# Optimization experiments

Hardware: AMD Instinct MI355X
Metric: run time of the kernel (lower is better)

The kernel has to match this reference:

```python
import jax, jax.numpy as jnp
import numpy as np

N, E, IN, H, F = 50000, 800000, 128, 4, 32
NEG_SLOPE = 0.2


def setup_inputs() -> dict:
    key = jax.random.key(0)
    ks = jax.random.split(key, 10)
    feat = jax.random.normal(ks[0], (N, IN), dtype=jnp.float32)
    s = 0.05  # small scale to keep activations stable
    W_src_mut = jax.random.normal(ks[1], (IN, H * F), dtype=jnp.float32) * s
    W_dst_mut = jax.random.normal(ks[2], (IN, H * F), dtype=jnp.float32) * s
    W_self = jax.random.normal(ks[3], (IN, H * F), dtype=jnp.float32) * s
    W_lin = jax.random.normal(ks[4], (IN, F), dtype=jnp.float32) * s
    attn = jax.random.normal(ks[5], (H, F), dtype=jnp.float32) * s
    src = jax.random.randint(ks[6], (E,), 0, N, dtype=jnp.int64)
    dst = jax.random.randint(ks[7], (E,), 0, N, dtype=jnp.int64)
    return {
        'feat': feat,
        'W_src_mut': W_src_mut, 'b_src_mut': jnp.zeros((H * F,), jnp.float32),
        'W_dst_mut': W_dst_mut, 'b_dst_mut': jnp.zeros((H * F,), jnp.float32),
        'W_self': W_self, 'b_self': jnp.zeros((H * F,), jnp.float32),
        'W_lin': W_lin, 'b_lin': jnp.zeros((F,), jnp.float32),
        'attn': attn, 'src': src, 'dst': dst,
    }


def reference(feat, W_src_mut, b_src_mut, W_dst_mut, b_dst_mut,
              W_self, b_self, W_lin, b_lin, attn, src, dst):
    n = feat.shape[0]
    # node projections -> [N, H, F]
    el_mut = (feat @ W_src_mut + b_src_mut).reshape(n, H, F)
    er_mut = (feat @ W_dst_mut + b_dst_mut).reshape(n, H, F)
    el_self = (feat @ W_self + b_self).reshape(n, H, F)
    feat_lin = (feat @ W_lin + b_lin)[:, None, :]  # [N, 1, F]
    # edge attention scores: u_add_v -> leaky_relu -> dot with attn -> [E, H]
    e = jax.nn.leaky_relu(el_mut[src] + er_mut[dst], NEG_SLOPE)
    s = jnp.einsum('ehf,hf->eh', e, attn)
    # edge softmax over incoming edges of each dst node
    smax = jax.ops.segment_max(s, dst, num_segments=n)
    ex = jnp.exp(s - smax[dst])
    denom = jax.ops.segment_sum(ex, dst, num_segments=n)
    a = ex / denom[dst]  # [E, H]
    # weighted aggregation: u_mul_e + sum over dst
    m = el_self[src] * a[:, :, None]  # [E, H, F]
    ft = jax.ops.segment_sum(m, dst, num_segments=n)  # [N, H, F]
    # concat along head axis: [N, H+1, F]
    return jnp.concatenate([feat_lin, ft], axis=1)
```

## Files before the change

### kernel.cpp

```cpp
#include <hip/hip_runtime.h>
#include <hip/hip_bf16.h>

#define NN 50000
#define EE 800000
#define INF_ 128
#define HH 4
#define FF 32
#define HF 128
#define OUTC 160
#define NEG_SLOPE 0.2f

#define SCAN_B 196

typedef __attribute__((ext_vector_type(8))) short short8;
typedef __attribute__((ext_vector_type(4))) float f32x4;
typedef _Float16 f16x2 __attribute__((ext_vector_type(2)));
typedef float fl2 __attribute__((ext_vector_type(2)));

__device__ __forceinline__ unsigned short f2bf(float f) {
    union { float f; unsigned u; } in; in.f = f;
    unsigned u = in.u;
    u += 0x7fffu + ((u >> 16) & 1u);
    return (unsigned short)(u >> 16);
}
__device__ __forceinline__ unsigned short f2h(float f) {
    _Float16 h = (_Float16)f;
    return __builtin_bit_cast(unsigned short, h);
}
__device__ __forceinline__ f16x2 bch(unsigned u) {
    return __builtin_bit_cast(f16x2, u);
}
__device__ __forceinline__ f16x2 habs2(f16x2 v) {
    unsigned u = __builtin_bit_cast(unsigned, v) & 0x7FFF7FFFu;
    return __builtin_bit_cast(f16x2, u);
}

__device__ __forceinline__ void async_cp16(const void* g, void* l) {
    __builtin_amdgcn_global_load_lds(
        (const __attribute__((address_space(1))) void*)g,
        (__attribute__((address_space(3))) void*)l, 16, 0, 0);
}

__global__ __launch_bounds__(256) void prep_w(
    const float* __restrict__ W0, const float* __restrict__ b0,
    const float* __restrict__ W1, const float* __restrict__ b1,
    const float* __restrict__ W2, const float* __restrict__ b2,
    const float* __restrict__ W3, const float* __restrict__ b3,
    const float* __restrict__ attn,
    unsigned short* __restrict__ WbT, float* __restrict__ biasc,
    unsigned short* __restrict__ ath)
{
    int idx = blockIdx.x * 256 + threadIdx.x;
    int n = idx >> 7, k = idx & 127;
    float v;
    if (n < 128)      v = W0[k * 128 + n];
    else if (n < 256) v = W1[k * 128 + (n - 128)];
    else if (n < 384) v = W2[k * 128 + (n - 256)];
    else              v = W3[k * 32  + (n - 384)];
    int phys = (((k >> 3) ^ (n & 15)) << 3) | (k & 7);
    WbT[n * 128 + phys] = f2bf(v);
    if (idx < 416) {
        float bv;
        if (idx < 128)      bv = b0[idx];
        else if (idx < 256) bv = b1[idx - 128];
        else if (idx < 384) bv = b2[idx - 256];
        else                bv = b3[idx - 384];
        biasc[idx] = bv;
    }
    if (idx < 128) ath[idx] = f2h(attn[idx]);
}

__global__ __launch_bounds__(256) void scan_bsum(
    const int* __restrict__ counts, int* __restrict__ bsum)
{
    __shared__ int sh[256];
    int t = threadIdx.x;
    int idx = blockIdx.x * 256 + t;
    sh[t] = (idx < NN) ? counts[idx] : 0;
    __syncthreads();
    #pragma unroll
    for (int off = 128; off > 0; off >>= 1) {
        if (t < off) sh[t] += sh[t + off];
        __syncthreads();
    }
    if (t == 0) bsum[blockIdx.x] = sh[0];
}

__global__ __launch_bounds__(256) void scan_top(
    const int* __restrict__ bsum, int* __restrict__ bprefix)
{
    __shared__ int sh[256];
    int t = threadIdx.x;
    int v = (t < SCAN_B) ? bsum[t] : 0;
    sh[t] = v;
    __syncthreads();
    #pragma unroll
    for (int off = 1; off < 256; off <<= 1) {
        int u = (t >= off) ? sh[t - off] : 0;
        __syncthreads();
        sh[t] += u;
        __syncthreads();
    }
    if (t < SCAN_B) bprefix[t] = sh[t] - v;
}

__global__ __launch_bounds__(256) void scan_final(
    const int* __restrict__ counts, const int* __restrict__ bprefix,
    int* __restrict__ offsets)
{
    __shared__ int sh[256];
    int t = threadIdx.x;
    int idx = blockIdx.x * 256 + t;
    int v = (idx < NN) ? counts[idx] : 0;
    sh[t] = v;
    __syncthreads();
    #pragma unroll
    for (int off = 1; off < 256; off <<= 1) {
        int u = (t >= off) ? sh[t - off] : 0;
        __syncthreads();
        sh[t] += u;
        __syncthreads();
    }
    if (idx < NN) offsets[idx] = sh[t] - v + bprefix[blockIdx.x];
}

__global__ void scatter_kernel(const int* __restrict__ src, const int* __restrict__ dst,
                               const int* __restrict__ offsets, const int* __restrict__ rank,
                               int* __restrict__ srcbuck)
{
    int e = blockIdx.x * blockDim.x + threadIdx.x;
    if (e < EE) srcbuck[offsets[dst[e]] + rank[e]] = src[e];
}


template<int CPR, int CSTR, int CA0>
__device__ __forceinline__ void copy_out(
    const unsigned short* Cs, int row0, int tid,
    unsigned short* __restrict__ muth, unsigned short* __restrict__ erh,
    unsigned short* __restrict__ selfh)
{
    for (int c = tid; c < 64 * CPR; c += 256) {
        int row = c / CPR, c16 = c - row * CPR;
        int grow = row0 + row;
        if (grow >= NN) continue;
        uint4 v = *(const uint4*)(Cs + row * CSTR + c16 * 8);
        int ca = CA0 + c16;
        if (ca < 16)      *(uint4*)(muth  + (size_t)grow * 128 + ca * 8) = v;
        else if (ca < 32) *(uint4*)(erh   + (size_t)grow * 128 + (ca - 16) * 8) = v;
        else              *(uint4*)(selfh + (size_t)grow * 128 + (ca - 32) * 8) = v;
    }
}

__global__ __launch_bounds__(256) void gemm_hist(
    const float* __restrict__ feat,
    const unsigned short* __restrict__ WbT,
    const float* __restrict__ biasc,
    const int* __restrict__ dst,
    unsigned short* __restrict__ muth, unsigned short* __restrict__ selfh,
    unsigned short* __restrict__ erh, float* __restrict__ out,
    int* __restrict__ counts, int* __restrict__ rank)
{
    __shared__ __align__(16) char lds[16384 + 28672];
    unsigned short* As = (unsigned short*)lds;
    unsigned short* Bs = (unsigned short*)(lds + 16384);
    unsigned short* Cs = (unsigned short*)lds;

    const int tid  = threadIdx.x;
    const int wv   = tid >> 6;
    const int lane = tid & 63;
    const int row0 = blockIdx.x * 64;
    const int yb   = blockIdx.y;

    {
        int e = (yb * 782 + blockIdx.x) * 256 + tid;
        if (e < EE) rank[e] = atomicAdd(&counts[dst[e]], 1);
    }

    const int ntile = (yb & 1) ? 6 : 7;
    const int base  = (yb == 0) ? 0 : (yb == 1) ? 112 : (yb == 2) ? 208 : 320;

    {
        const char* g = (const char*)(WbT + (size_t)base * 128);
        #pragma unroll
        for (int it = 0; it < 7; ++it) {
            if (it < ntile) {
                int seg = wv * ntile + it;
                async_cp16(g + seg * 1024 + lane * 16, (char*)Bs + seg * 1024);
            }
        }
    }
    {
        #pragma unroll
        for (int i = 0; i < 4; ++i) {
            int idx = i * 256 + tid;
            int r = idx >> 4, c = idx & 15;
            int grow = row0 + r;
            float4 v0 = make_float4(0.f, 0.f, 0.f, 0.f), v1 = v0;
            if (grow < NN) {
                const float4* fp = (const float4*)(feat + (size_t)grow * 128 + c * 8);
                v0 = fp[0]; v1 = fp[1];
            }
            uint4 o;
            o.x = (unsigned)f2bf(v0.x) | ((unsigned)f2bf(v0.y) << 16);
            o.y = (unsigned)f2bf(v0.z) | ((unsigned)f2bf(v0.w) << 16);
            o.z = (unsigned)f2bf(v1.x) | ((unsigned)f2bf(v1.y) << 16);
            o.w = (unsigned)f2bf(v1.z) | ((unsigned)f2bf(v1.w) << 16);
            *(uint4*)(As + r * 128 + ((c ^ (r & 15)) << 3)) = o;
        }
    }
    __syncthreads();

    const int m16  = lane & 15;
    const int quad = lane >> 4;

    f32x4 acc[7];
    #pragma unroll
    for (int t = 0; t < 7; ++t) acc[t] = (f32x4){0.f, 0.f, 0.f, 0.f};

    short8 afr[4];
    {
        const unsigned short* Ab = As + (wv * 16 + m16) * 128;
        #pragma unroll
        for (int ks = 0; ks < 4; ++ks)
            afr[ks] = *(const short8*)(Ab + (((ks * 4 + quad) ^ m16) << 3));
    }

    #pragma unroll
    for (int t = 0; t < 7; ++t) {
        if (t >= ntile) break;
        const unsigned short* Bb = Bs + (t * 16 + m16) * 128;
        #pragma unroll
        for (int ks = 0; ks < 4; ++ks) {
            short8 bfr = *(const short8*)(Bb + (((ks * 4 + quad) ^ m16) << 3));
            acc[t] = __builtin_amdgcn_mfma_f32_16x16x32_bf16(afr[ks], bfr, acc[t], 0, 0, 0);
        }
    }

    if (yb == 3) {
        #pragma unroll
        for (int t = 4; t < 6; ++t) {
            int col = 320 + t * 16 + m16;
            float bb = biasc[col];
            #pragma unroll
            for (int r = 0; r < 4; ++r) {
                int grow = row0 + wv * 16 + quad * 4 + r;
                if (grow < NN) out[(size_t)grow * OUTC + (col - 384)] = acc[t][r] + bb;
            }
        }
    }

    __syncthreads();

    const int ntf  = (yb == 3) ? 4 : ntile;
    const int cstr = (yb & 1) ? ((yb == 1) ? 104 : 72) : 120;
    #pragma unroll
    for (int t = 0; t < 7; ++t) {
        if (t >= ntf) break;
        int col = base + t * 16 + m16;
        float bb = biasc[col];
        #pragma unroll
        for (int r = 0; r < 4; ++r) {
            int lrow = wv * 16 + quad * 4 + r;
            Cs[lrow * cstr + t * 16 + m16] = f2h(acc[t][r] + bb);
        }
    }
    __syncthreads();

    if (yb == 0)      copy_out<14, 120, 0 >(Cs, row0, tid, muth, erh, selfh);
    else if (yb == 1) copy_out<12, 104, 14>(Cs, row0, tid, muth, erh, selfh);
    else if (yb == 2) copy_out<14, 120, 26>(Cs, row0, tid, muth, erh, selfh);
    else              copy_out<8,  72,  40>(Cs, row0, tid, muth, erh, selfh);
}

__device__ __forceinline__ void edgeP(
    const uint2 m, const uint2 sf, const f16x2 er01, const f16x2 er23,
    const f16x2 at01, const f16x2 at23,
    float& l, float& a0, float& a1, float& a2, float& a3)
{
    f16x2 z01 = bch(m.x) + er01;
    f16x2 z23 = bch(m.y) + er23;
    float s1 = __builtin_amdgcn_fdot2(at01, z01, 0.f, false);
    s1 = __builtin_amdgcn_fdot2(at23, z23, s1, false);
    float s2 = __builtin_amdgcn_fdot2(at01, habs2(z01), 0.f, false);
    s2 = __builtin_amdgcn_fdot2(at23, habs2(z23), s2, false);
    float s = fmaf(0.6f, s1, 0.4f * s2);
    s += __shfl_xor(s, 1, 64);
    s += __shfl_xor(s, 2, 64);
    s += __shfl_xor(s, 4, 64);
    float p = __expf(s);
    l += p;
    fl2 c01 = __builtin_convertvector(bch(sf.x), fl2);
    fl2 c23 = __builtin_convertvector(bch(sf.y), fl2);
    a0 = fmaf(p, c01.x, a0);
    a1 = fmaf(p, c01.y, a1);
    a2 = fmaf(p, c23.x, a2);
    a3 = fmaf(p, c23.y, a3);
}

__global__ __launch_bounds__(256) void node_agg5(
    const unsigned short* __restrict__ muth,
    const unsigned short* __restrict__ selfh,
    const unsigned short* __restrict__ erh,
    const unsigned short* __restrict__ ath,
    const int* __restrict__ offsets, const int* __restrict__ counts,
    const int* __restrict__ srcbuck, float* __restrict__ out)
{
    const int n = blockIdx.x * 4 + (threadIdx.x >> 6);
    if (n >= NN) return;
    const int lane = threadIdx.x & 63;
    const int half = lane >> 5;
    const int li   = lane & 31;

    uint2 aw = *(const uint2*)(ath + li * 4);
    uint2 ew = *(const uint2*)(erh + (size_t)n * HF + li * 4);
    const f16x2 at01 = bch(aw.x), at23 = bch(aw.y);
    const f16x2 er01 = bch(ew.x), er23 = bch(ew.y);

    const int beg = offsets[n];
    const int deg = counts[n];
    const int cnt0 = (deg + 1) >> 1;
    const int st  = beg + (half ? cnt0 : 0);
    const int cnt = half ? (deg - cnt0) : cnt0;

    float l = 0.f, a0 = 0.f, a1 = 0.f, a2 = 0.f, a3 = 0.f;

    int k = 0;
    for (; k + 4 <= cnt; k += 4) {
        int i0 = srcbuck[st + k];
        int i1 = srcbuck[st + k + 1];
        int i2 = srcbuck[st + k + 2];
        int i3 = srcbuck[st + k + 3];
        uint2 m0 = *(const uint2*)(muth + (size_t)i0 * HF + li * 4);
        uint2 m1 = *(const uint2*)(muth + (size_t)i1 * HF + li * 4);
        uint2 m2 = *(const uint2*)(muth + (size_t)i2 * HF + li * 4);
        uint2 m3 = *(const uint2*)(muth + (size_t)i3 * HF + li * 4);
        uint2 s0 = *(const uint2*)(selfh + (size_t)i0 * HF + li * 4);
        uint2 s1 = *(const uint2*)(selfh + (size_t)i1 * HF + li * 4);
        uint2 s2 = *(const uint2*)(selfh + (size_t)i2 * HF + li * 4);
        uint2 s3 = *(const uint2*)(selfh + (size_t)i3 * HF + li * 4);
        edgeP(m0, s0, er01, er23, at01, at23, l, a0, a1, a2, a3);
        edgeP(m1, s1, er01, er23, at01, at23, l, a0, a1, a2, a3);
        edgeP(m2, s2, er01, er23, at01, at23, l, a0, a1, a2, a3);
        edgeP(m3, s3, er01, er23, at01, at23, l, a0, a1, a2, a3);
    }
    for (; k < cnt; ++k) {
        int i0 = srcbuck[st + k];
        uint2 m0 = *(const uint2*)(muth + (size_t)i0 * HF + li * 4);
        uint2 s0 = *(const uint2*)(selfh + (size_t)i0 * HF + li * 4);
        edgeP(m0, s0, er01, er23, at01, at23, l, a0, a1, a2, a3);
    }

    l  += __shfl_xor(l,  32, 64);
    a0 += __shfl_xor(a0, 32, 64);
    a1 += __shfl_xor(a1, 32, 64);
    a2 += __shfl_xor(a2, 32, 64);
    a3 += __shfl_xor(a3, 32, 64);

    if (half == 0) {
        float inv = (l > 0.f) ? __frcp_rn(l) : 0.f;
        float4 r = make_float4(a0 * inv, a1 * inv, a2 * inv, a3 * inv);
        *(float4*)(out + (size_t)n * OUTC + FF + li * 4) = r;
    }
}

extern "C" void kernel_launch(void* const* d_in, const int* in_sizes, int n_in,
                              void* d_out, int out_size, void* d_ws, size_t ws_size,
                              hipStream_t stream) {
    const float* feat   = (const float*)d_in[0];
    const float* W_src  = (const float*)d_in[1];
    const float* b_src  = (const float*)d_in[2];
    const float* W_dst  = (const float*)d_in[3];
    const float* b_dst  = (const float*)d_in[4];
    const float* W_self = (const float*)d_in[5];
    const float* b_self = (const float*)d_in[6];
    const float* W_lin  = (const float*)d_in[7];
    const float* b_lin  = (const float*)d_in[8];
    const float* attn   = (const float*)d_in[9];
    const int*   src    = (const int*)d_in[10];
    const int*   dst    = (const int*)d_in[11];
    float* out = (float*)d_out;

    unsigned short* muth  = (unsigned short*)d_ws;
    unsigned short* selfh = muth  + (size_t)NN * HF;
    unsigned short* erh   = selfh + (size_t)NN * HF;
    unsigned short* WbT   = erh   + (size_t)NN * HF;
    unsigned short* ath   = WbT + 416 * 128;
    float* biasc   = (float*)(ath + 128);
    int*   counts  = (int*)(biasc + 416);
    int*   offsets = counts  + NN;
    int*   rank    = offsets + NN;
    int*   srcbuck = rank    + EE;
    int*   bsum    = srcbuck + EE;
    int*   bprefix = bsum    + SCAN_B;

    hipMemsetAsync(counts, 0, (size_t)NN * sizeof(int), stream);

    prep_w<<<208, 256, 0, stream>>>(W_src, b_src, W_dst, b_dst, W_self, b_self,
                                    W_lin, b_lin, attn, WbT, biasc, ath);

    {
        dim3 grid(782, 4);
        gemm_hist<<<grid, 256, 0, stream>>>(feat, WbT, biasc, dst,
                                            muth, selfh, erh, out, counts, rank);
    }

    scan_bsum <<<SCAN_B, 256, 0, stream>>>(counts, bsum);
    scan_top  <<<1, 256, 0, stream>>>(bsum, bprefix);
    scan_final<<<SCAN_B, 256, 0, stream>>>(counts, bprefix, offsets);
    scatter_kernel<<<(EE + 255) / 256, 256, 0, stream>>>(src, dst, offsets, rank, srcbuck);

    node_agg5<<<(NN + 3) / 4, 256, 0, stream>>>(muth, selfh, erh, ath,
                                                offsets, counts, srcbuck, out);
}
```

Baseline: 224.5 us.

## Interleave mut and self projections per node and fuse scan top into final

The src-side projections (mut and self) are written interleaved into one 256-halfword row per node, so each lane's gather in the aggregation kernel is a single 16-byte load instead of two 8-byte loads from separate arrays. Separately, the single-block top-level scan is removed: each final-scan block redundantly scans all block sums itself, saving one kernel launch. The cost is narrower uint2 stores in the GEMM epilogue and extra LDS scan work in every final-scan block.

```diff
diff --git a/kernel.cpp b/kernel.cpp
--- a/kernel.cpp
+++ b/kernel.cpp
@@ -86,42 +86,30 @@
     if (t == 0) bsum[blockIdx.x] = sh[0];
 }
 
-__global__ __launch_bounds__(256) void scan_top(
-    const int* __restrict__ bsum, int* __restrict__ bprefix)
+__global__ __launch_bounds__(256) void scan_final2(
+    const int* __restrict__ counts, const int* __restrict__ bsum,
+    int* __restrict__ offsets)
 {
     __shared__ int sh[256];
+    __shared__ int tops[256];
     int t = threadIdx.x;
-    int v = (t < SCAN_B) ? bsum[t] : 0;
-    sh[t] = v;
+    int idx = blockIdx.x * 256 + t;
+    int bv = (t < SCAN_B) ? bsum[t] : 0;
+    int v  = (idx < NN) ? counts[idx] : 0;
+    tops[t] = bv;
+    sh[t]   = v;
     __syncthreads();
     #pragma unroll
     for (int off = 1; off < 256; off <<= 1) {
-        int u = (t >= off) ? sh[t - off] : 0;
+        int u1 = (t >= off) ? sh[t - off] : 0;
+        int u2 = (t >= off) ? tops[t - off] : 0;
         __syncthreads();
-        sh[t] += u;
+        sh[t]   += u1;
+        tops[t] += u2;
         __syncthreads();
     }
-    if (t < SCAN_B) bprefix[t] = sh[t] - v;
-}
-
-__global__ __launch_bounds__(256) void scan_final(
-    const int* __restrict__ counts, const int* __restrict__ bprefix,
-    int* __restrict__ offsets)
-{
-    __shared__ int sh[256];
-    int t = threadIdx.x;
-    int idx = blockIdx.x * 256 + t;
-    int v = (idx < NN) ? counts[idx] : 0;
-    sh[t] = v;
-    __syncthreads();
-    #pragma unroll
-    for (int off = 1; off < 256; off <<= 1) {
-        int u = (t >= off) ? sh[t - off] : 0;
-        __syncthreads();
-        sh[t] += u;
-        __syncthreads();
-    }
-    if (idx < NN) offsets[idx] = sh[t] - v + bprefix[blockIdx.x];
+    int bpre = (blockIdx.x == 0) ? 0 : tops[blockIdx.x - 1];
+    if (idx < NN) offsets[idx] = sh[t] - v + bpre;
 }
 
 __global__ void scatter_kernel(const int* __restrict__ src, const int* __restrict__ dst,
@@ -136,8 +124,7 @@
 template<int CPR, int CSTR, int CA0>
 __device__ __forceinline__ void copy_out(
     const unsigned short* Cs, int row0, int tid,
-    unsigned short* __restrict__ muth, unsigned short* __restrict__ erh,
-    unsigned short* __restrict__ selfh)
+    unsigned short* __restrict__ ms, unsigned short* __restrict__ erh)
 {
     for (int c = tid; c < 64 * CPR; c += 256) {
         int row = c / CPR, c16 = c - row * CPR;
@@ -145,9 +132,18 @@
         if (grow >= NN) continue;
         uint4 v = *(const uint4*)(Cs + row * CSTR + c16 * 8);
         int ca = CA0 + c16;
-        if (ca < 16)      *(uint4*)(muth  + (size_t)grow * 128 + ca * 8) = v;
-        else if (ca < 32) *(uint4*)(erh   + (size_t)grow * 128 + (ca - 16) * 8) = v;
-        else              *(uint4*)(selfh + (size_t)grow * 128 + (ca - 32) * 8) = v;
+        if (ca < 16) {
+            unsigned short* p = ms + (size_t)grow * 256 + ca * 16;
+            *(uint2*)(p)     = make_uint2(v.x, v.y);
+            *(uint2*)(p + 8) = make_uint2(v.z, v.w);
+        } else if (ca < 32) {
+            *(uint4*)(erh + (size_t)grow * 128 + (ca - 16) * 8) = v;
+        } else {
+            int cs = ca - 32;
+            unsigned short* p = ms + (size_t)grow * 256 + cs * 16 + 4;
+            *(uint2*)(p)     = make_uint2(v.x, v.y);
+            *(uint2*)(p + 8) = make_uint2(v.z, v.w);
+        }
     }
 }
 
@@ -156,8 +152,8 @@
     const unsigned short* __restrict__ WbT,
     const float* __restrict__ biasc,
     const int* __restrict__ dst,
-    unsigned short* __restrict__ muth, unsigned short* __restrict__ selfh,
-    unsigned short* __restrict__ erh, float* __restrict__ out,
+    unsigned short* __restrict__ ms, unsigned short* __restrict__ erh,
+    float* __restrict__ out,
     int* __restrict__ counts, int* __restrict__ rank)
 {
     __shared__ __align__(16) char lds[16384 + 28672];
@@ -266,19 +262,19 @@
     }
     __syncthreads();
 
-    if (yb == 0)      copy_out<14, 120, 0 >(Cs, row0, tid, muth, erh, selfh);
-    else if (yb == 1) copy_out<12, 104, 14>(Cs, row0, tid, muth, erh, selfh);
-    else if (yb == 2) copy_out<14, 120, 26>(Cs, row0, tid, muth, erh, selfh);
-    else              copy_out<8,  72,  40>(Cs, row0, tid, muth, erh, selfh);
+    if (yb == 0)      copy_out<14, 120, 0 >(Cs, row0, tid, ms, erh);
+    else if (yb == 1) copy_out<12, 104, 14>(Cs, row0, tid, ms, erh);
+    else if (yb == 2) copy_out<14, 120, 26>(Cs, row0, tid, ms, erh);
+    else              copy_out<8,  72,  40>(Cs, row0, tid, ms, erh);
 }
 
 __device__ __forceinline__ void edgeP(
-    const uint2 m, const uint2 sf, const f16x2 er01, const f16x2 er23,
+    const uint4 v, const f16x2 er01, const f16x2 er23,
     const f16x2 at01, const f16x2 at23,
     float& l, float& a0, float& a1, float& a2, float& a3)
 {
-    f16x2 z01 = bch(m.x) + er01;
-    f16x2 z23 = bch(m.y) + er23;
+    f16x2 z01 = bch(v.x) + er01;
+    f16x2 z23 = bch(v.y) + er23;
     float s1 = __builtin_amdgcn_fdot2(at01, z01, 0.f, false);
     s1 = __builtin_amdgcn_fdot2(at23, z23, s1, false);
     float s2 = __builtin_amdgcn_fdot2(at01, habs2(z01), 0.f, false);
@@ -289,17 +285,16 @@
     s += __shfl_xor(s, 4, 64);
     float p = __expf(s);
     l += p;
-    fl2 c01 = __builtin_convertvector(bch(sf.x), fl2);
-    fl2 c23 = __builtin_convertvector(bch(sf.y), fl2);
+    fl2 c01 = __builtin_convertvector(bch(v.z), fl2);
+    fl2 c23 = __builtin_convertvector(bch(v.w), fl2);
     a0 = fmaf(p, c01.x, a0);
     a1 = fmaf(p, c01.y, a1);
     a2 = fmaf(p, c23.x, a2);
     a3 = fmaf(p, c23.y, a3);
 }
 
-__global__ __launch_bounds__(256) void node_agg5(
-    const unsigned short* __restrict__ muth,
-    const unsigned short* __restrict__ selfh,
+__global__ __launch_bounds__(256) void node_agg7(
+    const unsigned short* __restrict__ ms,
     const unsigned short* __restrict__ erh,
     const unsigned short* __restrict__ ath,
     const int* __restrict__ offsets, const int* __restrict__ counts,
@@ -330,24 +325,19 @@
         int i1 = srcbuck[st + k + 1];
         int i2 = srcbuck[st + k + 2];
         int i3 = srcbuck[st + k + 3];
-        uint2 m0 = *(const uint2*)(muth + (size_t)i0 * HF + li * 4);
-        uint2 m1 = *(const uint2*)(muth + (size_t)i1 * HF + li * 4);
-        uint2 m2 = *(const uint2*)(muth + (size_t)i2 * HF + li * 4);
-        uint2 m3 = *(const uint2*)(muth + (size_t)i3 * HF + li * 4);
-        uint2 s0 = *(const uint2*)(selfh + (size_t)i0 * HF + li * 4);
-        uint2 s1 = *(const uint2*)(selfh + (size_t)i1 * HF + li * 4);
-        uint2 s2 = *(const uint2*)(selfh + (size_t)i2 * HF + li * 4);
-        uint2 s3 = *(const uint2*)(selfh + (size_t)i3 * HF + li * 4);
-        edgeP(m0, s0, er01, er23, at01, at23, l, a0, a1, a2, a3);
-        edgeP(m1, s1, er01, er23, at01, at23, l, a0, a1, a2, a3);
-        edgeP(m2, s2, er01, er23, at01, at23, l, a0, a1, a2, a3);
-        edgeP(m3, s3, er01, er23, at01, at23, l, a0, a1, a2, a3);
+        uint4 v0 = *(const uint4*)(ms + (size_t)i0 * 256 + li * 8);
+        uint4 v1 = *(const uint4*)(ms + (size_t)i1 * 256 + li * 8);
+        uint4 v2 = *(const uint4*)(ms + (size_t)i2 * 256 + li * 8);
+        uint4 v3 = *(const uint4*)(ms + (size_t)i3 * 256 + li * 8);
+        edgeP(v0, er01, er23, at01, at23, l, a0, a1, a2, a3);
+        edgeP(v1, er01, er23, at01, at23, l, a0, a1, a2, a3);
+        edgeP(v2, er01, er23, at01, at23, l, a0, a1, a2, a3);
+        edgeP(v3, er01, er23, at01, at23, l, a0, a1, a2, a3);
     }
     for (; k < cnt; ++k) {
         int i0 = srcbuck[st + k];
-        uint2 m0 = *(const uint2*)(muth + (size_t)i0 * HF + li * 4);
-        uint2 s0 = *(const uint2*)(selfh + (size_t)i0 * HF + li * 4);
-        edgeP(m0, s0, er01, er23, at01, at23, l, a0, a1, a2, a3);
+        uint4 v0 = *(const uint4*)(ms + (size_t)i0 * 256 + li * 8);
+        edgeP(v0, er01, er23, at01, at23, l, a0, a1, a2, a3);
     }
 
     l  += __shfl_xor(l,  32, 64);
@@ -380,10 +370,9 @@
     const int*   dst    = (const int*)d_in[11];
     float* out = (float*)d_out;
 
-    unsigned short* muth  = (unsigned short*)d_ws;
-    unsigned short* selfh = muth  + (size_t)NN * HF;
-    unsigned short* erh   = selfh + (size_t)NN * HF;
-    unsigned short* WbT   = erh   + (size_t)NN * HF;
+    unsigned short* ms    = (unsigned short*)d_ws;
+    unsigned short* erh   = ms  + (size_t)NN * 256;
+    unsigned short* WbT   = erh + (size_t)NN * HF;
     unsigned short* ath   = WbT + 416 * 128;
     float* biasc   = (float*)(ath + 128);
     int*   counts  = (int*)(biasc + 416);
@@ -391,7 +380,6 @@
     int*   rank    = offsets + NN;
     int*   srcbuck = rank    + EE;
     int*   bsum    = srcbuck + EE;
-    int*   bprefix = bsum    + SCAN_B;
 
     hipMemsetAsync(counts, 0, (size_t)NN * sizeof(int), stream);
 
@@ -401,14 +389,13 @@
     {
         dim3 grid(782, 4);
         gemm_hist<<<grid, 256, 0, stream>>>(feat, WbT, biasc, dst,
-                                            muth, selfh, erh, out, counts, rank);
-    }
-
-    scan_bsum <<<SCAN_B, 256, 0, stream>>>(counts, bsum);
-    scan_top  <<<1, 256, 0, stream>>>(bsum, bprefix);
-    scan_final<<<SCAN_B, 256, 0, stream>>>(counts, bprefix, offsets);
+                                            ms, erh, out, counts, rank);
+    }
+
+    scan_bsum  <<<SCAN_B, 256, 0, stream>>>(counts, bsum);
+    scan_final2<<<SCAN_B, 256, 0, stream>>>(counts, bsum, offsets);
     scatter_kernel<<<(EE + 255) / 256, 256, 0, stream>>>(src, dst, offsets, rank, srcbuck);
 
-    node_agg5<<<(NN + 3) / 4, 256, 0, stream>>>(muth, selfh, erh, ath,
+    node_agg7<<<(NN + 3) / 4, 256, 0, stream>>>(ms, erh, ath,
                                                 offsets, counts, srcbuck, out);
 }
```

Result: faster. 219.2 us (-2.4%).
